# Optimization experiments

Hardware: AMD Instinct MI355X
Metric: run time of the kernel (lower is better)

Reference implementation:

```python
import jax, jax.numpy as jnp
import numpy as np

B, T, S, H, M, V, L = 16, 128, 256, 512, 512, 32000, 2


def setup_inputs() -> dict:
    key = jax.random.key(0)
    ks = jax.random.split(key, 16)
    s = 0.05
    embed = jax.random.normal(ks[3], (V, H), jnp.float32) * 0.02
    embed = embed.at[0].set(0.0)  # padding_idx=0 row is zero in nn.Embedding
    return {
        'tgt': jax.random.randint(ks[0], (B, T), 0, V),
        'hidden': jax.random.normal(ks[1], (L, B, M), jnp.float32) * 0.1,
        'enc_outs': jax.random.normal(ks[2], (B, S, M), jnp.float32) * 0.1,
        'embed': embed,
        'W_ih0': jax.random.normal(ks[4], (3 * M, H), jnp.float32) * s,
        'W_hh0': jax.random.normal(ks[5], (3 * M, M), jnp.float32) * s,
        'b_ih0': jax.random.normal(ks[6], (3 * M,), jnp.float32) * s,
        'b_hh0': jax.random.normal(ks[7], (3 * M,), jnp.float32) * s,
        'W_ih1': jax.random.normal(ks[8], (3 * M, M), jnp.float32) * s,
        'W_hh1': jax.random.normal(ks[9], (3 * M, M), jnp.float32) * s,
        'b_ih1': jax.random.normal(ks[10], (3 * M,), jnp.float32) * s,
        'b_hh1': jax.random.normal(ks[11], (3 * M,), jnp.float32) * s,
        'W_out': jax.random.normal(ks[12], (V, M), jnp.float32) * s,
        'b_out': jax.random.normal(ks[13], (V,), jnp.float32) * s,
    }


def _gru_layer(x, h0, W_ih, W_hh, b_ih, b_hh):
    """PyTorch-convention GRU layer. x: [B,T,in], h0: [B,M] -> (ys [B,T,M], hT [B,M])."""
    # precompute input-side gates for all timesteps: [B,T,3M]
    xg = jnp.einsum('bti,gi->btg', x, W_ih) + b_ih

    def step(h, xg_t):
        gh = h @ W_hh.T + b_hh
        i_r, i_z, i_n = jnp.split(xg_t, 3, axis=-1)
        h_r, h_z, h_n = jnp.split(gh, 3, axis=-1)
        r = jax.nn.sigmoid(i_r + h_r)
        z = jax.nn.sigmoid(i_z + h_z)
        n = jnp.tanh(i_n + r * h_n)
        h_new = (1.0 - z) * n + z * h
        return h_new, h_new

    hT, ys = jax.lax.scan(step, h0, jnp.swapaxes(xg, 0, 1))  # scan over time
    return jnp.swapaxes(ys, 0, 1), hT


def reference(tgt, hidden, enc_outs, embed, W_ih0, W_hh0, b_ih0, b_hh0,
              W_ih1, W_hh1, b_ih1, b_hh1, W_out, b_out):
    x = embed[tgt]  # [B,T,H]
    out0, h0f = _gru_layer(x, hidden[0], W_ih0, W_hh0, b_ih0, b_hh0)
    outputs, h1f = _gru_layer(out0, hidden[1], W_ih1, W_hh1, b_ih1, b_hh1)  # [B,T,M]
    hn = jnp.stack([h0f, h1f])  # [L,B,M]
    cn = jnp.zeros_like(hn)
    # dot-product attention, batched over all timesteps (fuses the per-ts Python loop)
    scores = jnp.einsum('btm,bsm->bts', outputs, enc_outs)
    weights = jax.nn.softmax(scores, axis=-1)
    contexts = jnp.einsum('bts,bsm->btm', weights, enc_outs)
    attn_outs = outputs + contexts
    logits = jnp.einsum('btm,vm->btv', attn_outs, W_out) + b_out  # dropout p=0 -> identity
    return logits, (hn, cn)
```

## Files before the change

### kernel.cpp

```cpp
#include <hip/hip_runtime.h>
#include <hip/hip_bf16.h>
#include <math.h>

#define B_ 16
#define T_ 128
#define S_ 256
#define H_ 512
#define M_ 512
#define V_ 32000
#define SENT 0x7FC0DEADu

typedef __attribute__((ext_vector_type(8))) short short8v;
typedef __attribute__((ext_vector_type(4))) float float4v;

__global__ __launch_bounds__(512) void k_fill(unsigned int* __restrict__ p, int n)
{
  const int i = blockIdx.x * 512 + threadIdx.x;
  if (i < n) p[i] = SENT;
}

__global__ __launch_bounds__(256) void k_xg_bf16(const int* __restrict__ tgt,
    const float* __restrict__ embed, const float* __restrict__ Bm,
    const float* __restrict__ bias, float* __restrict__ C)
{
  __shared__ unsigned short As[128 * 40];
  __shared__ unsigned short Bs[128 * 40];
  const int tid = threadIdx.x;
  const int nbase = blockIdx.x * 128;
  const int mbase = blockIdx.y * 128;
  const int wv = tid >> 6;
  const int l  = tid & 63;
  const int wr = wv >> 1, wc = wv & 1;
  const int r = l & 15, q = l >> 4;

  const int row0 = tid >> 2, row1 = (tid + 256) >> 2;
  const int v0 = tgt[mbase + row0];
  const int v1 = tgt[mbase + row1];

  float4v acc[4][4];
#pragma unroll
  for (int mi = 0; mi < 4; ++mi)
#pragma unroll
    for (int ni = 0; ni < 4; ++ni)
      acc[mi][ni] = (float4v){0.f, 0.f, 0.f, 0.f};

  for (int k0 = 0; k0 < 512; k0 += 32) {
    __syncthreads();
#pragma unroll
    for (int h = 0; h < 2; ++h) {
      const int c = tid + h * 256;
      const int row = h ? row1 : row0;
      const int av  = h ? v1 : v0;
      const int cb = c & 3;
      const float* Ag = embed + (size_t)av * 512 + k0 + cb * 8;
      float4 f0 = *(const float4*)(Ag);
      float4 f1 = *(const float4*)(Ag + 4);
      union { short8v v; __hip_bfloat162 h2[4]; } pa;
      pa.h2[0] = __float22bfloat162_rn({f0.x, f0.y});
      pa.h2[1] = __float22bfloat162_rn({f0.z, f0.w});
      pa.h2[2] = __float22bfloat162_rn({f1.x, f1.y});
      pa.h2[3] = __float22bfloat162_rn({f1.z, f1.w});
      *(short8v*)&As[row * 40 + cb * 8] = pa.v;
      const float* Bg = Bm + (size_t)(nbase + row) * 512 + k0 + cb * 8;
      float4 g0 = *(const float4*)(Bg);
      float4 g1 = *(const float4*)(Bg + 4);
      union { short8v v; __hip_bfloat162 h2[4]; } pb;
      pb.h2[0] = __float22bfloat162_rn({g0.x, g0.y});
      pb.h2[1] = __float22bfloat162_rn({g0.z, g0.w});
      pb.h2[2] = __float22bfloat162_rn({g1.x, g1.y});
      pb.h2[3] = __float22bfloat162_rn({g1.z, g1.w});
      *(short8v*)&Bs[row * 40 + cb * 8] = pb.v;
    }
    __syncthreads();

    short8v af[4], bf[4];
#pragma unroll
    for (int mi = 0; mi < 4; ++mi)
      af[mi] = *(short8v*)&As[(wr * 64 + mi * 16 + r) * 40 + q * 8];
#pragma unroll
    for (int ni = 0; ni < 4; ++ni)
      bf[ni] = *(short8v*)&Bs[(wc * 64 + ni * 16 + r) * 40 + q * 8];
#pragma unroll
    for (int mi = 0; mi < 4; ++mi)
#pragma unroll
      for (int ni = 0; ni < 4; ++ni)
        acc[mi][ni] = __builtin_amdgcn_mfma_f32_16x16x32_bf16(af[mi], bf[ni], acc[mi][ni], 0, 0, 0);
  }

  const int mg = mbase + wr * 64;
  const int ng = nbase + wc * 64;
#pragma unroll
  for (int ni = 0; ni < 4; ++ni) {
    const int col = ng + ni * 16 + r;
    const float bj = bias[col];
#pragma unroll
    for (int mi = 0; mi < 4; ++mi) {
      const int rowb = mg + mi * 16 + q * 4;
      float4v v = acc[mi][ni];
      C[(size_t)(rowb + 0) * 1536 + col] = v[0] + bj;
      C[(size_t)(rowb + 1) * 1536 + col] = v[1] + bj;
      C[(size_t)(rowb + 2) * 1536 + col] = v[2] + bj;
      C[(size_t)(rowb + 3) * 1536 + col] = v[3] + bj;
    }
  }
}

struct F4x8 { float4 a, b, c, d, e, f, g, h; };
__device__ inline F4x8 bulk8_ld(const float* rowbase, int sc)
{
  F4x8 r;
  const float* p = rowbase + sc * 4;
  asm volatile(
    "global_load_dwordx4 %0, %[p], off sc0 sc1\n\t"
    "global_load_dwordx4 %1, %[p], off offset:256 sc0 sc1\n\t"
    "global_load_dwordx4 %2, %[p], off offset:512 sc0 sc1\n\t"
    "global_load_dwordx4 %3, %[p], off offset:768 sc0 sc1\n\t"
    "global_load_dwordx4 %4, %[p], off offset:1024 sc0 sc1\n\t"
    "global_load_dwordx4 %5, %[p], off offset:1280 sc0 sc1\n\t"
    "global_load_dwordx4 %6, %[p], off offset:1536 sc0 sc1\n\t"
    "global_load_dwordx4 %7, %[p], off offset:1792 sc0 sc1\n\t"
    "s_waitcnt vmcnt(0)"
    : "=&v"(r.a), "=&v"(r.b), "=&v"(r.c), "=&v"(r.d),
      "=&v"(r.e), "=&v"(r.f), "=&v"(r.g), "=&v"(r.h)
    : [p]"v"(p)
    : "memory");
  return r;
}

__device__ inline void bulk16_ld(const float* r0base, const float* r1base, int sc,
                                 F4x8& x, F4x8& y)
{
  const float* p0 = r0base + sc * 4;
  const float* p1 = r1base + sc * 4;
  asm volatile(
    "global_load_dwordx4 %0, %[p0], off sc0 sc1\n\t"
    "global_load_dwordx4 %1, %[p0], off offset:256 sc0 sc1\n\t"
    "global_load_dwordx4 %2, %[p0], off offset:512 sc0 sc1\n\t"
    "global_load_dwordx4 %3, %[p0], off offset:768 sc0 sc1\n\t"
    "global_load_dwordx4 %4, %[p0], off offset:1024 sc0 sc1\n\t"
    "global_load_dwordx4 %5, %[p0], off offset:1280 sc0 sc1\n\t"
    "global_load_dwordx4 %6, %[p0], off offset:1536 sc0 sc1\n\t"
    "global_load_dwordx4 %7, %[p0], off offset:1792 sc0 sc1\n\t"
    "global_load_dwordx4 %8, %[p1], off sc0 sc1\n\t"
    "global_load_dwordx4 %9, %[p1], off offset:256 sc0 sc1\n\t"
    "global_load_dwordx4 %10, %[p1], off offset:512 sc0 sc1\n\t"
    "global_load_dwordx4 %11, %[p1], off offset:768 sc0 sc1\n\t"
    "global_load_dwordx4 %12, %[p1], off offset:1024 sc0 sc1\n\t"
    "global_load_dwordx4 %13, %[p1], off offset:1280 sc0 sc1\n\t"
    "global_load_dwordx4 %14, %[p1], off offset:1536 sc0 sc1\n\t"
    "global_load_dwordx4 %15, %[p1], off offset:1792 sc0 sc1\n\t"
    "s_waitcnt vmcnt(0)"
    : "=&v"(x.a), "=&v"(x.b), "=&v"(x.c), "=&v"(x.d),
      "=&v"(x.e), "=&v"(x.f), "=&v"(x.g), "=&v"(x.h),
      "=&v"(y.a), "=&v"(y.b), "=&v"(y.c), "=&v"(y.d),
      "=&v"(y.e), "=&v"(y.f), "=&v"(y.g), "=&v"(y.h)
    : [p0]"v"(p0), [p1]"v"(p1)
    : "memory");
}

__device__ inline bool anysent(const F4x8& r)
{
  auto c1 = [](float4 v) {
    return (__float_as_uint(v.x) == SENT) | (__float_as_uint(v.y) == SENT) |
           (__float_as_uint(v.z) == SENT) | (__float_as_uint(v.w) == SENT);
  };
  return c1(r.a) | c1(r.b) | c1(r.c) | c1(r.d) |
         c1(r.e) | c1(r.f) | c1(r.g) | c1(r.h);
}

__device__ inline void f4x8_store(const F4x8& r, int sc, float* dstrow)
{
  *(float4*)&dstrow[(0*16 + sc) * 4] = r.a;
  *(float4*)&dstrow[(1*16 + sc) * 4] = r.b;
  *(float4*)&dstrow[(2*16 + sc) * 4] = r.c;
  *(float4*)&dstrow[(3*16 + sc) * 4] = r.d;
  *(float4*)&dstrow[(4*16 + sc) * 4] = r.e;
  *(float4*)&dstrow[(5*16 + sc) * 4] = r.f;
  *(float4*)&dstrow[(6*16 + sc) * 4] = r.g;
  *(float4*)&dstrow[(7*16 + sc) * 4] = r.h;
}

__device__ inline void stage_sent(const float* rowbase, int sc, float* dstrow)
{
  F4x8 r = bulk8_ld(rowbase, sc);
  while (anysent(r)) {
    __builtin_amdgcn_s_sleep(1);
    r = bulk8_ld(rowbase, sc);
  }
  f4x8_store(r, sc, dstrow);
}

__device__ inline void stage2_sent(const float* r0base, const float* r1base,
                                   int sc, float* d0, float* d1)
{
  F4x8 x, y;
  bulk16_ld(r0base, r1base, sc, x, y);
  while (anysent(x)) {
    __builtin_amdgcn_s_sleep(1);
    x = bulk8_ld(r0base, sc);
  }
  f4x8_store(x, sc, d0);
  while (anysent(y)) {
    __builtin_amdgcn_s_sleep(1);
    y = bulk8_ld(r1base, sc);
  }
  f4x8_store(y, sc, d1);
}

__global__ __launch_bounds__(256) void k_gru2(
    const float* __restrict__ xg0,
    const float* __restrict__ Whh0, const float* __restrict__ bhh0,
    const float* __restrict__ Wih1, const float* __restrict__ bih1,
    const float* __restrict__ Whh1, const float* __restrict__ bhh1,
    const float* __restrict__ hidden,
    float* __restrict__ out0, float* __restrict__ y1, float* __restrict__ hn)
{
  __shared__ float Wl[24][520];
  __shared__ float hx[2][16 * 520];
  __shared__ float ps[24][16][17];
  const int bid = blockIdx.x;
  const int lt = threadIdx.x;

  if (bid >= 192) {
    __shared__ int done;
    if (lt == 0) done = 0;
    __syncthreads();
    const float* flag = y1 + (size_t)(15 * T_ + 127) * 512 + 511;
    float a0 = 1.0f + lt, a1 = 2.0f + lt, a2 = 3.0f, a3 = 4.0f;
    const float mb = 1.0001f, cb = 0.9999f;
    for (;;) {
#pragma unroll 16
      for (int i = 0; i < 512; ++i) {
        a0 = __builtin_fmaf(a0, mb, cb); a1 = __builtin_fmaf(a1, mb, cb);
        a2 = __builtin_fmaf(a2, mb, cb); a3 = __builtin_fmaf(a3, mb, cb);
      }
      if (lt == 0 &&
          __float_as_uint(__hip_atomic_load(flag, __ATOMIC_RELAXED,
                                            __HIP_MEMORY_SCOPE_AGENT)) != SENT)
        done = 1;
      __syncthreads();
      if (done) break;
    }
    asm volatile("" :: "v"(a0), "v"(a1), "v"(a2), "v"(a3));
    return;
  }

  const bool isB = bid >= 64;
  const int wg = isB ? bid - 64 : bid;
  const int dbase = isB ? wg * 4 : wg * 8;

  for (int r = 0; r < 24; ++r) {
    const float* src;
    if (!isB) src = Whh0 + (size_t)((r >> 3) * 512 + dbase + (r & 7)) * 512;
    else if (r < 12) src = Whh1 + (size_t)((r >> 2) * 512 + dbase + (r & 3)) * 512;
    else { int rr = r - 12; src = Wih1 + (size_t)((rr >> 2) * 512 + dbase + (rr & 3)) * 512; }
    Wl[r][lt] = src[lt];
    Wl[r][lt + 256] = src[lt + 256];
  }

  const int kq = lt & 15;
  const int bq = (lt >> 4) & 3;
  const int rgrp = lt >> 6;
  const int sb = lt >> 4;
  const int sc = lt & 15;
  float* ybuf = isB ? y1 : out0;
  const float* h0g = hidden + (isB ? 8192 : 0);

  const int rb = isB ? (lt >> 2) : (lt >> 3);
  const int rdl = isB ? (lt & 3) : (lt & 7);
  const int rdg = dbase + rdl;
  const int nred = isB ? 64 : 128;
  float bhr = 0.f, bhz = 0.f, bhn = 0.f, bir = 0.f, biz = 0.f, bin_ = 0.f;
  if (lt < nred) {
    const float* bhh = isB ? bhh1 : bhh0;
    bhr = bhh[rdg]; bhz = bhh[512 + rdg]; bhn = bhh[1024 + rdg];
    if (isB) { bir = bih1[rdg]; biz = bih1[512 + rdg]; bin_ = bih1[1024 + rdg]; }
  }
  __syncthreads();

  for (int t = 0; t < T_; ++t) {
    float pxr = 0.f, pxz = 0.f, pxn = 0.f;
    if (!isB && lt < 128) {
      const float* xrow = xg0 + (size_t)(rb * T_ + t) * 1536;
      pxr = xrow[rdg]; pxz = xrow[512 + rdg]; pxn = xrow[1024 + rdg];
    }

    if (t == 0) {
#pragma unroll
      for (int j = 0; j < 8; ++j)
        *(float4*)&hx[0][sb * 520 + (j * 16 + sc) * 4] =
            *(const float4*)(h0g + sb * 512 + (j * 16 + sc) * 4);
      if (isB)
        stage_sent(out0 + (size_t)(sb * T_) * 512, sc, &hx[1][sb * 520]);
    } else if (!isB) {
      stage_sent(ybuf + (size_t)(sb * T_ + t - 1) * 512, sc, &hx[0][sb * 520]);
    } else {
      stage2_sent(ybuf + (size_t)(sb * T_ + t - 1) * 512,
                  out0 + (size_t)(sb * T_ + t) * 512,
                  sc, &hx[0][sb * 520], &hx[1][sb * 520]);
    }
    __syncthreads();

    const float* inb = (isB && rgrp >= 2) ? &hx[1][0] : &hx[0][0];
    float acc[6][4];
#pragma unroll
    for (int jr = 0; jr < 6; ++jr)
#pragma unroll
      for (int jb = 0; jb < 4; ++jb) acc[jr][jb] = 0.f;
#pragma unroll
    for (int i = 0; i < 8; ++i) {
      const int kb = kq * 4 + i * 64;
      float4 hv0 = *(const float4*)(inb + (bq * 4 + 0) * 520 + kb);
      float4 hv1 = *(const float4*)(inb + (bq * 4 + 1) * 520 + kb);
      float4 hv2 = *(const float4*)(inb + (bq * 4 + 2) * 520 + kb);
      float4 hv3 = *(const float4*)(inb + (bq * 4 + 3) * 520 + kb);
#pragma unroll
      for (int jr = 0; jr < 6; ++jr) {
        float4 wv = *(const float4*)(&Wl[rgrp * 6 + jr][kb]);
        acc[jr][0] += wv.x*hv0.x + wv.y*hv0.y + wv.z*hv0.z + wv.w*hv0.w;
        acc[jr][1] += wv.x*hv1.x + wv.y*hv1.y + wv.z*hv1.z + wv.w*hv1.w;
        acc[jr][2] += wv.x*hv2.x + wv.y*hv2.y + wv.z*hv2.z + wv.w*hv2.w;
        acc[jr][3] += wv.x*hv3.x + wv.y*hv3.y + wv.z*hv3.z + wv.w*hv3.w;
      }
    }
#pragma unroll
    for (int jr = 0; jr < 6; ++jr)
#pragma unroll
      for (int jb = 0; jb < 4; ++jb)
        ps[rgrp * 6 + jr][bq * 4 + jb][kq] = acc[jr][jb];
    __syncthreads();

    if (lt < nred) {
      float ghr, ghz, ghn, ixr, ixz, ixn;
      if (!isB) {
        float s0 = 0.f, s1 = 0.f, s2 = 0.f;
#pragma unroll
        for (int q = 0; q < 16; ++q) {
          s0 += ps[rdl][rb][q];
          s1 += ps[8 + rdl][rb][q];
          s2 += ps[16 + rdl][rb][q];
        }
        ghr = s0 + bhr; ghz = s1 + bhz; ghn = s2 + bhn;
        ixr = pxr; ixz = pxz; ixn = pxn;
      } else {
        float s0=0.f,s1=0.f,s2=0.f,s3=0.f,s4=0.f,s5=0.f;
#pragma unroll
        for (int q = 0; q < 16; ++q) {
          s0 += ps[rdl][rb][q];       s1 += ps[4 + rdl][rb][q];  s2 += ps[8 + rdl][rb][q];
          s3 += ps[12 + rdl][rb][q];  s4 += ps[16 + rdl][rb][q]; s5 += ps[20 + rdl][rb][q];
        }
        ghr = s0 + bhr; ghz = s1 + bhz; ghn = s2 + bhn;
        ixr = s3 + bir; ixz = s4 + biz; ixn = s5 + bin_;
      }
      float rr = 1.f / (1.f + expf(-(ixr + ghr)));
      float zz = 1.f / (1.f + expf(-(ixz + ghz)));
      float nn = tanhf(ixn + rr * ghn);
      float hp = hx[0][rb * 520 + rdg];
      float hnew = (1.f - zz) * nn + zz * hp;
      __hip_atomic_store(&ybuf[(size_t)(rb * T_ + t) * 512 + rdg], hnew,
                         __ATOMIC_RELAXED, __HIP_MEMORY_SCOPE_AGENT);
      if (t == T_ - 1) hn[(isB ? 8192 : 0) + rb * 512 + rdg] = hnew;
    }
    __syncthreads();
  }
}

__global__ __launch_bounds__(256) void k_attn(const float* __restrict__ y,
    const float* __restrict__ enc, float* __restrict__ aout)
{
  __shared__ float orow[512];
  __shared__ float wbuf[256];
  __shared__ float red[8];
  const int row = blockIdx.x;
  const int b = row >> 7;
  const int lt = threadIdx.x;
  orow[lt]       = y[(size_t)row*512 + lt];
  orow[lt + 256] = y[(size_t)row*512 + lt + 256];
  __syncthreads();
  const float* er = enc + (size_t)(b*S_ + lt) * 512;
  float acc = 0.f;
  for (int k = 0; k < 512; k += 4) {
    float4 e = *(const float4*)(er + k);
    acc += orow[k]*e.x + orow[k+1]*e.y + orow[k+2]*e.z + orow[k+3]*e.w;
  }
  float m = acc;
#pragma unroll
  for (int off = 32; off > 0; off >>= 1) m = fmaxf(m, __shfl_down(m, off));
  if ((lt & 63) == 0) red[lt >> 6] = m;
  __syncthreads();
  float mx = fmaxf(fmaxf(red[0], red[1]), fmaxf(red[2], red[3]));
  float e = expf(acc - mx);
  wbuf[lt] = e;
  float s = e;
#pragma unroll
  for (int off = 32; off > 0; off >>= 1) s += __shfl_down(s, off);
  if ((lt & 63) == 0) red[4 + (lt >> 6)] = s;
  __syncthreads();
  const float inv = 1.f / (red[4] + red[5] + red[6] + red[7]);
  const int kk = lt * 2;
  float c0 = 0.f, c1 = 0.f;
  for (int s2 = 0; s2 < S_; ++s2) {
    float ws = wbuf[s2];
    float2 ev = *(const float2*)(enc + (size_t)(b*S_ + s2)*512 + kk);
    c0 += ws * ev.x; c1 += ws * ev.y;
  }
  aout[(size_t)row*512 + kk]     = orow[kk]     + c0 * inv;
  aout[(size_t)row*512 + kk + 1] = orow[kk + 1] + c1 * inv;
}

__global__ __launch_bounds__(256) void k_logits(const float* __restrict__ A,
    const float* __restrict__ Bm, const float* __restrict__ bias,
    float* __restrict__ C)
{
  __shared__ unsigned short Bs[128 * 512];
  __shared__ unsigned short As[128 * 64];
  const int tid = threadIdx.x;
  const int nbase = blockIdx.x * 128;
  const int wv = tid >> 6;
  const int l  = tid & 63;
  const int wr = wv >> 1, wc = wv & 1;
  const int r = l & 15, q = l >> 4;

  for (int i = 0; i < 32; ++i) {
    const int gid = tid + i * 256;
    const int row = gid >> 6, cg = gid & 63;
    const float* Bg = Bm + (size_t)(nbase + row) * 512 + cg * 8;
    float4 g0 = *(const float4*)(Bg);
    float4 g1 = *(const float4*)(Bg + 4);
    union { short8v v; __hip_bfloat162 h2[4]; } pb;
    pb.h2[0] = __float22bfloat162_rn({g0.x, g0.y});
    pb.h2[1] = __float22bfloat162_rn({g0.z, g0.w});
    pb.h2[2] = __float22bfloat162_rn({g1.x, g1.y});
    pb.h2[3] = __float22bfloat162_rn({g1.z, g1.w});
    const int byte = (row * 1024 + cg * 16) ^ ((row & 7) << 4);
    *(short8v*)&Bs[byte >> 1] = pb.v;
  }
  __syncthreads();

  for (int m = 0; m < 16; ++m) {
    const int mbase = m * 128;
    float4v acc[4][4];
#pragma unroll
    for (int mi = 0; mi < 4; ++mi)
#pragma unroll
      for (int ni = 0; ni < 4; ++ni)
        acc[mi][ni] = (float4v){0.f, 0.f, 0.f, 0.f};

    for (int kc = 0; kc < 8; ++kc) {
#pragma unroll
      for (int i = 0; i < 4; ++i) {
        const int gid = tid + i * 256;
        const int row = gid >> 3, cg = gid & 7;
        const float* Ag = A + (size_t)(mbase + row) * 512 + kc * 64 + cg * 8;
        float4 f0 = *(const float4*)(Ag);
        float4 f1 = *(const float4*)(Ag + 4);
        union { short8v v; __hip_bfloat162 h2[4]; } pa;
        pa.h2[0] = __float22bfloat162_rn({f0.x, f0.y});
        pa.h2[1] = __float22bfloat162_rn({f0.z, f0.w});
        pa.h2[2] = __float22bfloat162_rn({f1.x, f1.y});
        pa.h2[3] = __float22bfloat162_rn({f1.z, f1.w});
        const int byte = (row * 128 + cg * 16) ^ ((row & 7) << 4);
        *(short8v*)&As[byte >> 1] = pa.v;
      }
      __syncthreads();

#pragma unroll
      for (int k0s = 0; k0s < 2; ++k0s) {
        short8v af[4], bf[4];
#pragma unroll
        for (int mi = 0; mi < 4; ++mi) {
          const int row = wr * 64 + mi * 16 + r;
          const int byte = (row * 128 + k0s * 64 + q * 16) ^ ((row & 7) << 4);
          af[mi] = *(short8v*)&As[byte >> 1];
        }
#pragma unroll
        for (int ni = 0; ni < 4; ++ni) {
          const int row = wc * 64 + ni * 16 + r;
          const int byte = (row * 1024 + kc * 128 + k0s * 64 + q * 16) ^ ((row & 7) << 4);
          bf[ni] = *(short8v*)&Bs[byte >> 1];
        }
#pragma unroll
        for (int mi = 0; mi < 4; ++mi)
#pragma unroll
          for (int ni = 0; ni < 4; ++ni)
            acc[mi][ni] = __builtin_amdgcn_mfma_f32_16x16x32_bf16(af[mi], bf[ni], acc[mi][ni], 0, 0, 0);
      }
      __syncthreads();
    }

    const int mg = mbase + wr * 64;
    const int ng = nbase + wc * 64;
#pragma unroll
    for (int ni = 0; ni < 4; ++ni) {
      const int col = ng + ni * 16 + r;
      const float bj = bias[col];
#pragma unroll
      for (int mi = 0; mi < 4; ++mi) {
        const int rowb = mg + mi * 16 + q * 4;
        float4v v = acc[mi][ni];
        C[(size_t)(rowb + 0) * V_ + col] = v[0] + bj;
        C[(size_t)(rowb + 1) * V_ + col] = v[1] + bj;
        C[(size_t)(rowb + 2) * V_ + col] = v[2] + bj;
        C[(size_t)(rowb + 3) * V_ + col] = v[3] + bj;
      }
    }
  }
}

extern "C" void kernel_launch(void* const* d_in, const int* in_sizes, int n_in,
                              void* d_out, int out_size, void* d_ws, size_t ws_size,
                              hipStream_t stream)
{
  const int*   tgt    = (const int*)  d_in[0];
  const float* hidden = (const float*)d_in[1];
  const float* enc    = (const float*)d_in[2];
  const float* embed  = (const float*)d_in[3];
  const float* W_ih0  = (const float*)d_in[4];
  const float* W_hh0  = (const float*)d_in[5];
  const float* b_ih0  = (const float*)d_in[6];
  const float* b_hh0  = (const float*)d_in[7];
  const float* W_ih1  = (const float*)d_in[8];
  const float* W_hh1  = (const float*)d_in[9];
  const float* b_ih1  = (const float*)d_in[10];
  const float* b_hh1  = (const float*)d_in[11];
  const float* W_out  = (const float*)d_in[12];
  const float* b_out  = (const float*)d_in[13];
  float* out = (float*)d_out;

  float* ws   = (float*)d_ws;
  float* xbuf = ws;
  float* xg   = ws + 1048576;
  float* out0 = xg + 3145728;
  float* y1   = out0 + 1048576;

  const size_t logitsN = (size_t)(B_*T_) * V_;
  float* hn = out + logitsN;
  float* cn = hn + 16384;

  hipMemsetAsync(cn, 0, (size_t)16384 * sizeof(float), stream);

  k_fill<<<dim3(4096), dim3(512), 0, stream>>>((unsigned int*)out0, 2097152);
  k_xg_bf16<<<dim3(1536/128, 2048/128), dim3(256), 0, stream>>>(tgt, embed, W_ih0, b_ih0, xg);
  k_gru2<<<dim3(256), dim3(256), 0, stream>>>(xg, W_hh0, b_hh0, W_ih1, b_ih1,
                                              W_hh1, b_hh1, hidden, out0, y1, hn);
  k_attn<<<dim3(B_*T_), dim3(256), 0, stream>>>(y1, enc, xbuf);
  k_logits<<<dim3(V_/128), dim3(256), 0, stream>>>(xbuf, W_out, b_out, out);
}
```

Measured before the change: 1.305 ms.

## Cache GRU weights in registers, emit bf16 attention outputs, prefetch A tiles

In the recurrent GRU kernel, each thread now loads its slice of the hidden-to-hidden weights from shared memory into registers once, instead of rereading it every timestep. The hidden-state row stride changes to 524 to alter the LDS bank pattern, and the kernel is capped at one block per CU. The attention kernel now writes bf16 directly, so the logits GEMM loads pre-converted A tiles and software-prefetches the next k-chunk into registers while MFMAs run. The costs are heavy register pressure (48 float4 per thread), which risks spills, plus an extra barrier per k-chunk.

New measurement: 1.294 ms. About the same (-0.8%).

```diff
diff --git a/kernel.cpp b/kernel.cpp
--- a/kernel.cpp
+++ b/kernel.cpp
@@ -9,6 +9,7 @@
 #define M_ 512
 #define V_ 32000
 #define SENT 0x7FC0DEADu
+#define HPAD 524
 
 typedef __attribute__((ext_vector_type(8))) short short8v;
 typedef __attribute__((ext_vector_type(4))) float float4v;
@@ -207,7 +208,7 @@
   f4x8_store(y, sc, d1);
 }
 
-__global__ __launch_bounds__(256) void k_gru2(
+__global__ __launch_bounds__(256, 1) void k_gru2(
     const float* __restrict__ xg0,
     const float* __restrict__ Whh0, const float* __restrict__ bhh0,
     const float* __restrict__ Wih1, const float* __restrict__ bih1,
@@ -216,7 +217,7 @@
     float* __restrict__ out0, float* __restrict__ y1, float* __restrict__ hn)
 {
   __shared__ float Wl[24][520];
-  __shared__ float hx[2][16 * 520];
+  __shared__ float hx[2][16 * HPAD];
   __shared__ float ps[24][16][17];
   const int bid = blockIdx.x;
   const int lt = threadIdx.x;
@@ -278,6 +279,13 @@
   }
   __syncthreads();
 
+  float4 wreg[6][8];
+#pragma unroll
+  for (int jr = 0; jr < 6; ++jr)
+#pragma unroll
+    for (int i = 0; i < 8; ++i)
+      wreg[jr][i] = *(const float4*)(&Wl[rgrp * 6 + jr][kq * 4 + i * 64]);
+
   for (int t = 0; t < T_; ++t) {
     float pxr = 0.f, pxz = 0.f, pxn = 0.f;
     if (!isB && lt < 128) {
@@ -288,16 +296,16 @@
     if (t == 0) {
 #pragma unroll
       for (int j = 0; j < 8; ++j)
-        *(float4*)&hx[0][sb * 520 + (j * 16 + sc) * 4] =
+        *(float4*)&hx[0][sb * HPAD + (j * 16 + sc) * 4] =
             *(const float4*)(h0g + sb * 512 + (j * 16 + sc) * 4);
       if (isB)
-        stage_sent(out0 + (size_t)(sb * T_) * 512, sc, &hx[1][sb * 520]);
+        stage_sent(out0 + (size_t)(sb * T_) * 512, sc, &hx[1][sb * HPAD]);
     } else if (!isB) {
-      stage_sent(ybuf + (size_t)(sb * T_ + t - 1) * 512, sc, &hx[0][sb * 520]);
+      stage_sent(ybuf + (size_t)(sb * T_ + t - 1) * 512, sc, &hx[0][sb * HPAD]);
     } else {
       stage2_sent(ybuf + (size_t)(sb * T_ + t - 1) * 512,
                   out0 + (size_t)(sb * T_ + t) * 512,
-                  sc, &hx[0][sb * 520], &hx[1][sb * 520]);
+                  sc, &hx[0][sb * HPAD], &hx[1][sb * HPAD]);
     }
     __syncthreads();
 
@@ -310,13 +318,13 @@
 #pragma unroll
     for (int i = 0; i < 8; ++i) {
       const int kb = kq * 4 + i * 64;
-      float4 hv0 = *(const float4*)(inb + (bq * 4 + 0) * 520 + kb);
-      float4 hv1 = *(const float4*)(inb + (bq * 4 + 1) * 520 + kb);
-      float4 hv2 = *(const float4*)(inb + (bq * 4 + 2) * 520 + kb);
-      float4 hv3 = *(const float4*)(inb + (bq * 4 + 3) * 520 + kb);
+      float4 hv0 = *(const float4*)(inb + (bq * 4 + 0) * HPAD + kb);
+      float4 hv1 = *(const float4*)(inb + (bq * 4 + 1) * HPAD + kb);
+      float4 hv2 = *(const float4*)(inb + (bq * 4 + 2) * HPAD + kb);
+      float4 hv3 = *(const float4*)(inb + (bq * 4 + 3) * HPAD + kb);
 #pragma unroll
       for (int jr = 0; jr < 6; ++jr) {
-        float4 wv = *(const float4*)(&Wl[rgrp * 6 + jr][kb]);
+        float4 wv = wreg[jr][i];
         acc[jr][0] += wv.x*hv0.x + wv.y*hv0.y + wv.z*hv0.z + wv.w*hv0.w;
         acc[jr][1] += wv.x*hv1.x + wv.y*hv1.y + wv.z*hv1.z + wv.w*hv1.w;
         acc[jr][2] += wv.x*hv2.x + wv.y*hv2.y + wv.z*hv2.z + wv.w*hv2.w;
@@ -355,7 +363,7 @@
       float rr = 1.f / (1.f + expf(-(ixr + ghr)));
       float zz = 1.f / (1.f + expf(-(ixz + ghz)));
       float nn = tanhf(ixn + rr * ghn);
-      float hp = hx[0][rb * 520 + rdg];
+      float hp = hx[0][rb * HPAD + rdg];
       float hnew = (1.f - zz) * nn + zz * hp;
       __hip_atomic_store(&ybuf[(size_t)(rb * T_ + t) * 512 + rdg], hnew,
                          __ATOMIC_RELAXED, __HIP_MEMORY_SCOPE_AGENT);
@@ -366,7 +374,7 @@
 }
 
 __global__ __launch_bounds__(256) void k_attn(const float* __restrict__ y,
-    const float* __restrict__ enc, float* __restrict__ aout)
+    const float* __restrict__ enc, __hip_bfloat162* __restrict__ abf)
 {
   __shared__ float orow[512];
   __shared__ float wbuf[256];
@@ -404,11 +412,11 @@
     float2 ev = *(const float2*)(enc + (size_t)(b*S_ + s2)*512 + kk);
     c0 += ws * ev.x; c1 += ws * ev.y;
   }
-  aout[(size_t)row*512 + kk]     = orow[kk]     + c0 * inv;
-  aout[(size_t)row*512 + kk + 1] = orow[kk + 1] + c1 * inv;
-}
-
-__global__ __launch_bounds__(256) void k_logits(const float* __restrict__ A,
+  abf[(size_t)row * 256 + lt] =
+      __float22bfloat162_rn({orow[kk] + c0 * inv, orow[kk + 1] + c1 * inv});
+}
+
+__global__ __launch_bounds__(256) void k_logits(const unsigned short* __restrict__ Abf,
     const float* __restrict__ Bm, const float* __restrict__ bias,
     float* __restrict__ C)
 {
@@ -435,6 +443,14 @@
     const int byte = (row * 1024 + cg * 16) ^ ((row & 7) << 4);
     *(short8v*)&Bs[byte >> 1] = pb.v;
   }
+
+  int arow[4], acg[4], abyte[4];
+#pragma unroll
+  for (int i = 0; i < 4; ++i) {
+    const int gid = tid + i * 256;
+    arow[i] = gid >> 3; acg[i] = gid & 7;
+    abyte[i] = (arow[i] * 128 + acg[i] * 16) ^ ((arow[i] & 7) << 4);
+  }
   __syncthreads();
 
   for (int m = 0; m < 16; ++m) {
@@ -446,23 +462,26 @@
       for (int ni = 0; ni < 4; ++ni)
         acc[mi][ni] = (float4v){0.f, 0.f, 0.f, 0.f};
 
+    {
+      short8v a0[4];
+#pragma unroll
+      for (int i = 0; i < 4; ++i)
+        a0[i] = *(const short8v*)(Abf + (size_t)(mbase + arow[i]) * 512 + acg[i] * 8);
+      __syncthreads();
+#pragma unroll
+      for (int i = 0; i < 4; ++i)
+        *(short8v*)&As[abyte[i] >> 1] = a0[i];
+      __syncthreads();
+    }
+
     for (int kc = 0; kc < 8; ++kc) {
-#pragma unroll
-      for (int i = 0; i < 4; ++i) {
-        const int gid = tid + i * 256;
-        const int row = gid >> 3, cg = gid & 7;
-        const float* Ag = A + (size_t)(mbase + row) * 512 + kc * 64 + cg * 8;
-        float4 f0 = *(const float4*)(Ag);
-        float4 f1 = *(const float4*)(Ag + 4);
-        union { short8v v; __hip_bfloat162 h2[4]; } pa;
-        pa.h2[0] = __float22bfloat162_rn({f0.x, f0.y});
-        pa.h2[1] = __float22bfloat162_rn({f0.z, f0.w});
-        pa.h2[2] = __float22bfloat162_rn({f1.x, f1.y});
-        pa.h2[3] = __float22bfloat162_rn({f1.z, f1.w});
-        const int byte = (row * 128 + cg * 16) ^ ((row & 7) << 4);
-        *(short8v*)&As[byte >> 1] = pa.v;
-      }
-      __syncthreads();
+      short8v anext[4];
+      if (kc < 7) {
+#pragma unroll
+        for (int i = 0; i < 4; ++i)
+          anext[i] = *(const short8v*)(Abf + (size_t)(mbase + arow[i]) * 512 +
+                                       (kc + 1) * 64 + acg[i] * 8);
+      }
 
 #pragma unroll
       for (int k0s = 0; k0s < 2; ++k0s) {
@@ -484,6 +503,12 @@
 #pragma unroll
           for (int ni = 0; ni < 4; ++ni)
             acc[mi][ni] = __builtin_amdgcn_mfma_f32_16x16x32_bf16(af[mi], bf[ni], acc[mi][ni], 0, 0, 0);
+      }
+      __syncthreads();
+      if (kc < 7) {
+#pragma unroll
+        for (int i = 0; i < 4; ++i)
+          *(short8v*)&As[abyte[i] >> 1] = anext[i];
       }
       __syncthreads();
     }
@@ -528,7 +553,7 @@
   float* out = (float*)d_out;
 
   float* ws   = (float*)d_ws;
-  float* xbuf = ws;
+  __hip_bfloat162* abf = (__hip_bfloat162*)ws;
   float* xg   = ws + 1048576;
   float* out0 = xg + 3145728;
   float* y1   = out0 + 1048576;
@@ -543,6 +568,7 @@
   k_xg_bf16<<<dim3(1536/128, 2048/128), dim3(256), 0, stream>>>(tgt, embed, W_ih0, b_ih0, xg);
   k_gru2<<<dim3(256), dim3(256), 0, stream>>>(xg, W_hh0, b_hh0, W_ih1, b_ih1,
                                               W_hh1, b_hh1, hidden, out0, y1, hn);
-  k_attn<<<dim3(B_*T_), dim3(256), 0, stream>>>(y1, enc, xbuf);
-  k_logits<<<dim3(V_/128), dim3(256), 0, stream>>>(xbuf, W_out, b_out, out);
-}
+  k_attn<<<dim3(B_*T_), dim3(256), 0, stream>>>(y1, enc, abf);
+  k_logits<<<dim3(V_/128), dim3(256), 0, stream>>>((const unsigned short*)abf,
+                                                   W_out, b_out, out);
+}
```
